# Kernel optimization log

Hardware: AMD Instinct MI355X
Metric: run time of the kernel (lower is better)

## Reference

```python
import jax, jax.numpy as jnp
import numpy as np

N, D, H, C = 100000, 128, 8, 16  # nodes, units=H*C, heads, per-head channels
E = 400000                        # edges per edge set (2 edge sets)
LN_EPS = 1e-3                     # keras LayerNormalization default epsilon


def setup_inputs() -> dict:
    key = jax.random.key(0)
    ks = jax.random.split(key, 16)
    def dense(k, i, o):
        return jax.random.normal(k, (i, o), jnp.float32) / np.float32(np.sqrt(i))
    return dict(
        x=jax.random.normal(ks[0], (N, D), jnp.float32),
        src0=jax.random.randint(ks[1], (E,), 0, N),
        dst0=jax.random.randint(ks[2], (E,), 0, N),
        src1=jax.random.randint(ks[3], (E,), 0, N),
        dst1=jax.random.randint(ks[4], (E,), 0, N),
        Wk=dense(ks[5], D, D), bk=jnp.zeros((D,), jnp.float32),
        Wm=dense(ks[6], D, D), bm=jnp.zeros((D,), jnp.float32),
        Wq=dense(ks[7], D, D), bq=jnp.zeros((D,), jnp.float32),
        Wa=dense(ks[8], D, D), ba=jnp.zeros((D,), jnp.float32),
        Watt0=jax.random.normal(ks[9], (H, C, C), jnp.float32) / np.float32(np.sqrt(C)),
        Wmsg0=jax.random.normal(ks[10], (H, C, C), jnp.float32) / np.float32(np.sqrt(C)),
        Watt1=jax.random.normal(ks[11], (H, C, C), jnp.float32) / np.float32(np.sqrt(C)),
        Wmsg1=jax.random.normal(ks[12], (H, C, C), jnp.float32) / np.float32(np.sqrt(C)),
        prior0=jnp.ones((H,), jnp.float32),
        prior1=jnp.ones((H,), jnp.float32),
        skip=jnp.ones((), jnp.float32),
        gamma=jnp.ones((D,), jnp.float32),
        beta=jnp.zeros((D,), jnp.float32),
    )


def reference(x, src0, dst0, src1, dst1, Wk, bk, Wm, bm, Wq, bq, Wa, ba,
              Watt0, Wmsg0, Watt1, Wmsg1, prior0, prior1, skip, gamma, beta):
    # Node-level projections, split per head: [N, H, C]
    k = (x @ Wk + bk).reshape(N, H, C)
    m = (x @ Wm + bm).reshape(N, H, C)
    q = (x @ Wq + bq).reshape(N, H, C)
    scale = 1.0 / jnp.sqrt(jnp.float32(C))

    def edge_terms(src, dst, Watt, Wmsg, prior):
        # per-edge-type relation projections of gathered sender keys/messages
        ke = jnp.einsum('ehk,hkl->ehl', k[src], Watt)          # [E, H, C]
        score = jnp.einsum('ehl,ehl->eh', ke, q[dst]) * prior * scale  # [E, H]
        msg = jnp.einsum('ehk,hkl->ehl', m[src], Wmsg)          # [E, H, C]
        return score, msg

    s0, m0 = edge_terms(src0, dst0, Watt0, Wmsg0, prior0)
    s1, m1 = edge_terms(src1, dst1, Watt1, Wmsg1, prior1)

    # Joint segment softmax over all incoming edges (both edge sets) per receiver
    scores = jnp.concatenate([s0, s1], axis=0)   # [2E, H]
    msgs = jnp.concatenate([m0, m1], axis=0)     # [2E, H, C]
    recv = jnp.concatenate([dst0, dst1], axis=0)

    smax = jax.ops.segment_max(scores, recv, num_segments=N)   # [N, H]
    ex = jnp.exp(scores - smax[recv])
    denom = jax.ops.segment_sum(ex, recv, num_segments=N)      # [N, H]
    d_e = denom[recv]
    attn = ex / jnp.where(d_e > 0, d_e, 1.0)                   # [2E, H]

    pooled = jax.ops.segment_sum(attn[:, :, None] * msgs, recv,
                                 num_segments=N).reshape(N, D)  # [N, D]

    # aggr(gelu(pooled)); weighted skip; layer norm
    h = jax.nn.gelu(pooled, approximate=False) @ Wa + ba
    alpha = jax.nn.sigmoid(skip)
    out = alpha * h + (1.0 - alpha) * x
    mu = jnp.mean(out, axis=-1, keepdims=True)
    var = jnp.var(out, axis=-1, keepdims=True)
    out = (out - mu) * jax.lax.rsqrt(var + LN_EPS) * gamma + beta
    return out
```

## Files before the change

kernel.cpp:

```cpp
#include <hip/hip_runtime.h>
#include <hip/hip_bf16.h>
#include <math.h>

#define N_NODES 100000
#define DIM 128
#define NH 8
#define NC 16
#define E_EDGES 400000
#define LN_EPS 1e-3f
#define SCAN_B 1024
#define PROJ_GRID 512

typedef __attribute__((ext_vector_type(8))) short short8v;
typedef __attribute__((ext_vector_type(4))) short short4v;
typedef __attribute__((ext_vector_type(4))) float float4v;

__device__ __forceinline__ short bf16bits(float v) {
    __hip_bfloat16 b = __float2bfloat16(v);
    return *(short*)&b;
}

__device__ __forceinline__ void bf2x2(unsigned v, float& a, float& b) {
    a = __uint_as_float(v << 16);
    b = __uint_as_float(v & 0xffff0000u);
}

__global__ __launch_bounds__(128) void fuse_weights(
    const float* __restrict__ Wk, const float* __restrict__ bk,
    const float* __restrict__ Wm, const float* __restrict__ bm,
    const float* __restrict__ Wq, const float* __restrict__ bq,
    const float* __restrict__ Wa, const float* __restrict__ ba,
    const float* __restrict__ Watt0, const float* __restrict__ Wmsg0,
    const float* __restrict__ Watt1, const float* __restrict__ Wmsg1,
    const float* __restrict__ prior0, const float* __restrict__ prior1,
    __hip_bfloat16* __restrict__ Wt, float* __restrict__ bias)
{
    const int c = blockIdx.x;
    const int d = threadIdx.x;
    const int sec = c >> 7, j = c & 127, h = j >> 4, l = j & 15;
    float v = 0.f, b = 0.f;
    if (sec == 0)      { v = Wk[d * DIM + j]; b = bk[j]; }
    else if (sec == 1) { v = Wm[d * DIM + j]; b = bm[j]; }
    else if (sec == 4) { v = Wa[d * DIM + j]; b = ba[j]; }
    else if (sec == 2 || sec == 3) {
        const float* W2 = (sec == 2) ? Watt0 : Watt1;
        float scale = ((sec == 2) ? prior0[h] : prior1[h]) * 0.25f;
        float s = 0.f, sb = 0.f;
        #pragma unroll
        for (int ll = 0; ll < NC; ++ll) {
            float w2 = W2[h * 256 + l * 16 + ll];
            s  = fmaf(Wq[d * DIM + h * 16 + ll], w2, s);
            sb = fmaf(bq[h * 16 + ll], w2, sb);
        }
        v = s * scale; b = sb * scale;
    } else {
        const float* W2 = (sec == 5) ? Wmsg0 : Wmsg1;
        v = ((d >> 4) == h) ? W2[h * 256 + (d & 15) * 16 + l] : 0.f;
        b = 0.f;
    }
    Wt[(size_t)c * DIM + d] = __float2bfloat16(v);
    if (d == 0) bias[c] = b;
}

__global__ __launch_bounds__(512) void proj_mfma(
    const float* __restrict__ x,
    const __hip_bfloat16* __restrict__ Wt,
    const float* __restrict__ bias,
    __hip_bfloat16* __restrict__ kmr,
    __hip_bfloat16* __restrict__ qe)
{
    __shared__ __align__(16) short xs[2][32 * DIM];
    const int tid = threadIdx.x;
    const int wave = tid >> 6, lane = tid & 63;
    const int quad = lane >> 4, mcol = lane & 15;
    const int nt = N_NODES / 32;

    short8v wf[4][4];
    float4v bv[4];
    #pragma unroll
    for (int s = 0; s < 4; ++s) {
        const int c0 = s * 128 + wave * 16;
        const short* wp = (const short*)Wt + (size_t)(c0 + mcol) * DIM + quad * 8;
        #pragma unroll
        for (int kb = 0; kb < 4; ++kb)
            wf[s][kb] = *(const short8v*)(wp + kb * 32);
        bv[s] = *(const float4v*)(bias + c0 + quad * 4);
    }

    const int srow = tid >> 4, sc8 = tid & 15;
    const int swz = ((sc8 ^ (srow & 7)) * 8);

    int t = blockIdx.x;
    if (t >= nt) return;

    float4v f0 = *(const float4v*)(x + (size_t)(t * 32 + srow) * DIM + sc8 * 8);
    float4v f1 = *(const float4v*)(x + (size_t)(t * 32 + srow) * DIM + sc8 * 8 + 4);
    {
        short8v sv;
        #pragma unroll
        for (int j = 0; j < 4; ++j) { sv[j] = bf16bits(f0[j]); sv[j + 4] = bf16bits(f1[j]); }
        *(short8v*)(xs[0] + srow * DIM + swz) = sv;
    }
    {
        int nn = t + PROJ_GRID;
        if (nn < nt) {
            f0 = *(const float4v*)(x + (size_t)(nn * 32 + srow) * DIM + sc8 * 8);
            f1 = *(const float4v*)(x + (size_t)(nn * 32 + srow) * DIM + sc8 * 8 + 4);
        }
    }

    int cur = 0;
    for (; t < nt; t += PROJ_GRID) {
        asm volatile("s_waitcnt lgkmcnt(0)" ::: "memory");
        __builtin_amdgcn_s_barrier();

        short8v b0[4], b1[4];
        #pragma unroll
        for (int kb = 0; kb < 4; ++kb) {
            const int ch = ((quad + kb * 4) ^ (mcol & 7)) * 8;
            b0[kb] = *(const short8v*)(xs[cur] + mcol * DIM + ch);
            b1[kb] = *(const short8v*)(xs[cur] + (mcol + 16) * DIM + ch);
        }

        const int r0 = t * 32;

        {
            float4v aK0 = {0.f,0.f,0.f,0.f}, aK1 = {0.f,0.f,0.f,0.f};
            float4v aM0 = {0.f,0.f,0.f,0.f}, aM1 = {0.f,0.f,0.f,0.f};
            #pragma unroll
            for (int kb = 0; kb < 4; ++kb) {
                aK0 = __builtin_amdgcn_mfma_f32_16x16x32_bf16(wf[0][kb], b0[kb], aK0, 0, 0, 0);
                aK1 = __builtin_amdgcn_mfma_f32_16x16x32_bf16(wf[0][kb], b1[kb], aK1, 0, 0, 0);
                aM0 = __builtin_amdgcn_mfma_f32_16x16x32_bf16(wf[1][kb], b0[kb], aM0, 0, 0, 0);
                aM1 = __builtin_amdgcn_mfma_f32_16x16x32_bf16(wf[1][kb], b1[kb], aM1, 0, 0, 0);
            }
            short8v o0, o1;
            #pragma unroll
            for (int g = 0; g < 4; ++g) {
                o0[g]     = bf16bits(aK0[g] + bv[0][g]);
                o0[g + 4] = bf16bits(aM0[g] + bv[1][g]);
                o1[g]     = bf16bits(aK1[g] + bv[0][g]);
                o1[g + 4] = bf16bits(aM1[g] + bv[1][g]);
            }
            short* dp = (short*)kmr + (size_t)(r0 + mcol) * 256
                      + (wave * 4 + quad) * 8;
            *(short8v*)dp              = o0;
            *(short8v*)(dp + 16 * 256) = o1;
        }

        #pragma unroll
        for (int e = 0; e < 2; ++e) {
            float4v a0v = {0.f,0.f,0.f,0.f}, a1v = {0.f,0.f,0.f,0.f};
            #pragma unroll
            for (int kb = 0; kb < 4; ++kb) {
                a0v = __builtin_amdgcn_mfma_f32_16x16x32_bf16(wf[2 + e][kb], b0[kb], a0v, 0, 0, 0);
                a1v = __builtin_amdgcn_mfma_f32_16x16x32_bf16(wf[2 + e][kb], b1[kb], a1v, 0, 0, 0);
            }
            short4v o0, o1;
            #pragma unroll
            for (int g = 0; g < 4; ++g) {
                o0[g] = bf16bits(a0v[g] + bv[2 + e][g]);
                o1[g] = bf16bits(a1v[g] + bv[2 + e][g]);
            }
            short* dp = (short*)qe + ((size_t)e * N_NODES + r0 + mcol) * DIM
                      + wave * 16 + quad * 4;
            *(short4v*)dp              = o0;
            *(short4v*)(dp + 16 * DIM) = o1;
        }

        int nn = t + PROJ_GRID;
        if (nn < nt) {
            short8v sv;
            #pragma unroll
            for (int j = 0; j < 4; ++j) { sv[j] = bf16bits(f0[j]); sv[j + 4] = bf16bits(f1[j]); }
            *(short8v*)(xs[cur ^ 1] + srow * DIM + swz) = sv;
            int n2 = nn + PROJ_GRID;
            if (n2 < nt) {
                f0 = *(const float4v*)(x + (size_t)(n2 * 32 + srow) * DIM + sc8 * 8);
                f1 = *(const float4v*)(x + (size_t)(n2 * 32 + srow) * DIM + sc8 * 8 + 4);
            }
        }
        cur ^= 1;
    }
}

__global__ __launch_bounds__(256) void hist_kernel(
    const int* __restrict__ dst0, const int* __restrict__ dst1,
    int* __restrict__ counts)
{
    int e = blockIdx.x * 256 + threadIdx.x;
    if (e < E_EDGES) atomicAdd(&counts[dst0[e]], 1);
    int e1 = e - E_EDGES;
    if (e1 >= 0 && e1 < E_EDGES) atomicAdd(&counts[dst1[e1]], 1);
}

__global__ __launch_bounds__(SCAN_B) void scanA_kernel(
    const int* __restrict__ counts, int* __restrict__ row_ptr,
    int* __restrict__ bsum)
{
    __shared__ int buf[2][SCAN_B];
    int i = blockIdx.x * SCAN_B + threadIdx.x;
    int v = (i < N_NODES) ? counts[i] : 0;
    int cur = 0;
    buf[0][threadIdx.x] = v;
    __syncthreads();
    #pragma unroll
    for (int off = 1; off < SCAN_B; off <<= 1) {
        int t = buf[cur][threadIdx.x];
        int add = (threadIdx.x >= off) ? buf[cur][threadIdx.x - off] : 0;
        buf[cur ^ 1][threadIdx.x] = t + add;
        cur ^= 1;
        __syncthreads();
    }
    int inc = buf[cur][threadIdx.x];
    if (i < N_NODES) row_ptr[i] = inc - v;
    if (threadIdx.x == SCAN_B - 1) bsum[blockIdx.x] = inc;
}

__global__ __launch_bounds__(128) void scanB_kernel(int* __restrict__ bsum, int nblocks)
{
    __shared__ int buf[2][128];
    int t = threadIdx.x;
    int v = (t < nblocks) ? bsum[t] : 0;
    buf[0][t] = v;
    __syncthreads();
    int cur = 0;
    #pragma unroll
    for (int off = 1; off < 128; off <<= 1) {
        int a = buf[cur][t];
        if (t >= off) a += buf[cur][t - off];
        buf[cur ^ 1][t] = a;
        cur ^= 1;
        __syncthreads();
    }
    if (t < nblocks) bsum[t] = buf[cur][t] - v;
}

__global__ __launch_bounds__(SCAN_B) void scanC_kernel(
    int* __restrict__ row_ptr, int* __restrict__ cursor,
    const int* __restrict__ bsum)
{
    int i = blockIdx.x * SCAN_B + threadIdx.x;
    if (i < N_NODES) {
        int r = row_ptr[i] + bsum[blockIdx.x];
        row_ptr[i] = r;
        cursor[i] = r;
    }
}

__global__ __launch_bounds__(256) void scatter_kernel(
    const int* __restrict__ src0, const int* __restrict__ dst0,
    const int* __restrict__ src1, const int* __restrict__ dst1,
    int* __restrict__ cursor, unsigned int* __restrict__ eidx)
{
    int e = blockIdx.x * 256 + threadIdx.x;
    if (e < E_EDGES) {
        int d = dst0[e];
        int pos = atomicAdd(&cursor[d], 1);
        eidx[pos] = (unsigned int)src0[e];
    }
    int e1 = e - E_EDGES;
    if (e1 >= 0 && e1 < E_EDGES) {
        int d = dst1[e1];
        int pos = atomicAdd(&cursor[d], 1);
        eidx[pos] = (unsigned int)src1[e1] | 0x80000000u;
    }
}

__global__ __launch_bounds__(256) void agg_kernel(
    const char* __restrict__ kmr,
    const uint2* __restrict__ qe,
    const int* __restrict__ row_ptr, const int* __restrict__ counts,
    const unsigned int* __restrict__ eidx,
    __hip_bfloat16* __restrict__ acc)
{
    const int wave = threadIdx.x >> 6, lane = threadIdx.x & 63;
    const int n = blockIdx.x * 4 + wave;
    if (n >= N_NODES) return;
    const int start = row_ptr[n], cnt = counts[n];
    const int hi = lane >> 5;
    const int glane = lane & 31;
    const unsigned g16 = (unsigned)glane << 4;

    uint2 qu0 = qe[(size_t)n * 32 + glane];
    uint2 qu1 = qe[((size_t)N_NODES + n) * 32 + glane];
    float q00, q01, q02, q03, q10, q11, q12, q13;
    bf2x2(qu0.x, q00, q01); bf2x2(qu0.y, q02, q03);
    bf2x2(qu1.x, q10, q11); bf2x2(qu1.y, q12, q13);

    float b0 = 0.f, b1 = 0.f, b2 = 0.f, b3 = 0.f;
    float c0 = 0.f, c1 = 0.f, c2 = 0.f, c3 = 0.f;
    float den = 0.f;

#define PAIR_ACC(u, s1)                                                      \
    {                                                                        \
        float k0, k1, k2, k3, m0, m1, m2, m3;                                \
        bf2x2((u).x, k0, k1); bf2x2((u).y, k2, k3);                          \
        bf2x2((u).z, m0, m1); bf2x2((u).w, m2, m3);                          \
        float qa = (s1) ? q10 : q00, qb = (s1) ? q11 : q01;                  \
        float qc = (s1) ? q12 : q02, qd = (s1) ? q13 : q03;                  \
        float p = fmaf(k3, qd, fmaf(k2, qc, fmaf(k1, qb, k0 * qa)));         \
        p += __shfl_xor(p, 1, 64);                                           \
        p += __shfl_xor(p, 2, 64);                                           \
        float e = __expf(p);                                                 \
        den += e;                                                            \
        float e0 = (s1) ? 0.f : e, e1s = (s1) ? e : 0.f;                     \
        b0 = fmaf(e0, m0, b0); b1 = fmaf(e0, m1, b1);                        \
        b2 = fmaf(e0, m2, b2); b3 = fmaf(e0, m3, b3);                        \
        c0 = fmaf(e1s, m0, c0); c1 = fmaf(e1s, m1, c1);                      \
        c2 = fmaf(e1s, m2, c2); c3 = fmaf(e1s, m3, c3);                      \
    }

    int i = 0;
    for (; i + 8 <= cnt; i += 8) {
        unsigned ra = eidx[start + i + hi];
        unsigned rb = eidx[start + i + 2 + hi];
        unsigned rc = eidx[start + i + 4 + hi];
        unsigned rd = eidx[start + i + 6 + hi];
        uint4 ua = *(const uint4*)(kmr + ((size_t)(ra & 0x7fffffffu) << 9 | g16));
        uint4 ub = *(const uint4*)(kmr + ((size_t)(rb & 0x7fffffffu) << 9 | g16));
        uint4 uc = *(const uint4*)(kmr + ((size_t)(rc & 0x7fffffffu) << 9 | g16));
        uint4 ud = *(const uint4*)(kmr + ((size_t)(rd & 0x7fffffffu) << 9 | g16));
        PAIR_ACC(ua, (ra >> 31));
        PAIR_ACC(ub, (rb >> 31));
        PAIR_ACC(uc, (rc >> 31));
        PAIR_ACC(ud, (rd >> 31));
    }
    for (; i + 2 <= cnt; i += 2) {
        unsigned ra = eidx[start + i + hi];
        uint4 ua = *(const uint4*)(kmr + ((size_t)(ra & 0x7fffffffu) << 9 | g16));
        PAIR_ACC(ua, (ra >> 31));
    }
    if (i < cnt) {
        unsigned ra = eidx[start + i];
        uint4 ua = *(const uint4*)(kmr + ((size_t)(ra & 0x7fffffffu) << 9 | g16));
        unsigned s1 = ra >> 31;
        float k0, k1, k2, k3, m0, m1, m2, m3;
        bf2x2(ua.x, k0, k1); bf2x2(ua.y, k2, k3);
        bf2x2(ua.z, m0, m1); bf2x2(ua.w, m2, m3);
        float qa = s1 ? q10 : q00, qb = s1 ? q11 : q01;
        float qc = s1 ? q12 : q02, qd = s1 ? q13 : q03;
        float p = fmaf(k3, qd, fmaf(k2, qc, fmaf(k1, qb, k0 * qa)));
        p += __shfl_xor(p, 1, 64);
        p += __shfl_xor(p, 2, 64);
        float e = hi ? 0.f : __expf(p);
        den += e;
        float e0 = s1 ? 0.f : e, e1s = s1 ? e : 0.f;
        b0 = fmaf(e0, m0, b0); b1 = fmaf(e0, m1, b1);
        b2 = fmaf(e0, m2, b2); b3 = fmaf(e0, m3, b3);
        c0 = fmaf(e1s, m0, c0); c1 = fmaf(e1s, m1, c1);
        c2 = fmaf(e1s, m2, c2); c3 = fmaf(e1s, m3, c3);
    }
#undef PAIR_ACC

    den += __shfl_xor(den, 32, 64);
    b0 += __shfl_xor(b0, 32, 64); b1 += __shfl_xor(b1, 32, 64);
    b2 += __shfl_xor(b2, 32, 64); b3 += __shfl_xor(b3, 32, 64);
    c0 += __shfl_xor(c0, 32, 64); c1 += __shfl_xor(c1, 32, 64);
    c2 += __shfl_xor(c2, 32, 64); c3 += __shfl_xor(c3, 32, 64);

    float inv = (den > 0.f) ? (1.f / den) : 0.f;
    short4v o;
    if (!hi) {
        o[0] = bf16bits(b0 * inv); o[1] = bf16bits(b1 * inv);
        o[2] = bf16bits(b2 * inv); o[3] = bf16bits(b3 * inv);
        *(short4v*)((short*)acc + (size_t)n * 256 + glane * 4) = o;
    } else {
        o[0] = bf16bits(c0 * inv); o[1] = bf16bits(c1 * inv);
        o[2] = bf16bits(c2 * inv); o[3] = bf16bits(c3 * inv);
        *(short4v*)((short*)acc + (size_t)n * 256 + 128 + glane * 4) = o;
    }
}

__global__ __launch_bounds__(256) void final_mfma(
    const __hip_bfloat16* __restrict__ acc,
    const __hip_bfloat16* __restrict__ Wt,
    const float* __restrict__ bias,
    const float* __restrict__ x,
    const float* __restrict__ skip, const float* __restrict__ gamma,
    const float* __restrict__ beta, float* __restrict__ out)
{
    __shared__ __align__(16) short Pl[32 * DIM];
    __shared__ float hs[32][DIM];
    const int wave = threadIdx.x >> 6, lane = threadIdx.x & 63;
    const int quad = lane >> 4, mcol = lane & 15;
    const int r0 = blockIdx.x * 32;

    short8v a0[8], a1[8];
    const short* pp0 = (const short*)acc + (size_t)(r0 + mcol) * 256 + quad * 8;
    const short* pp1 = pp0 + 16 * 256;
    #pragma unroll
    for (int kb = 0; kb < 8; ++kb) {
        a0[kb] = *(const short8v*)(pp0 + kb * 32);
        a1[kb] = *(const short8v*)(pp1 + kb * 32);
    }
    const float alpha = 1.f / (1.f + expf(-skip[0]));

    #pragma unroll
    for (int t = 0; t < 2; ++t) {
        const int c0 = wave * 32 + t * 16;
        const short* wp5 = (const short*)Wt + (size_t)(5 * 128 + c0 + mcol) * DIM + quad * 8;
        const short* wp6 = (const short*)Wt + (size_t)(6 * 128 + c0 + mcol) * DIM + quad * 8;
        float4v p0 = {0.f, 0.f, 0.f, 0.f};
        float4v p1 = {0.f, 0.f, 0.f, 0.f};
        #pragma unroll
        for (int kb = 0; kb < 4; ++kb) {
            short8v bfr = *(const short8v*)(wp5 + kb * 32);
            p0 = __builtin_amdgcn_mfma_f32_16x16x32_bf16(a0[kb], bfr, p0, 0, 0, 0);
            p1 = __builtin_amdgcn_mfma_f32_16x16x32_bf16(a1[kb], bfr, p1, 0, 0, 0);
        }
        #pragma unroll
        for (int kb = 0; kb < 4; ++kb) {
            short8v bfr = *(const short8v*)(wp6 + kb * 32);
            p0 = __builtin_amdgcn_mfma_f32_16x16x32_bf16(a0[kb + 4], bfr, p0, 0, 0, 0);
            p1 = __builtin_amdgcn_mfma_f32_16x16x32_bf16(a1[kb + 4], bfr, p1, 0, 0, 0);
        }
        const int cc = c0 + mcol;
        #pragma unroll
        for (int g = 0; g < 4; ++g) {
            int rA = quad * 4 + g, rB = rA + 16;
            float vA = p0[g], vB = p1[g];
            vA = 0.5f * vA * (1.f + erff(vA * 0.70710678118654752f));
            vB = 0.5f * vB * (1.f + erff(vB * 0.70710678118654752f));
            Pl[rA * DIM + (((cc >> 3) ^ (rA & 7)) << 3) + (cc & 7)] = bf16bits(vA);
            Pl[rB * DIM + (((cc >> 3) ^ (rB & 7)) << 3) + (cc & 7)] = bf16bits(vB);
        }
    }
    __syncthreads();

    short8v g0[4], g1[4];
    #pragma unroll
    for (int kb = 0; kb < 4; ++kb) {
        const int ch = quad + kb * 4;
        g0[kb] = *(const short8v*)(Pl + mcol * DIM + ((ch ^ (mcol & 7)) << 3));
        g1[kb] = *(const short8v*)(Pl + (mcol + 16) * DIM + ((ch ^ (mcol & 7)) << 3));
    }

    #pragma unroll
    for (int t = 0; t < 2; ++t) {
        const int c0 = wave * 32 + t * 16;
        const short* wp = (const short*)Wt + (size_t)(4 * 128 + c0 + mcol) * DIM + quad * 8;
        float4v acc0 = {0.f, 0.f, 0.f, 0.f};
        float4v acc1 = {0.f, 0.f, 0.f, 0.f};
        #pragma unroll
        for (int kb = 0; kb < 4; ++kb) {
            short8v bfr = *(const short8v*)(wp + kb * 32);
            acc0 = __builtin_amdgcn_mfma_f32_16x16x32_bf16(g0[kb], bfr, acc0, 0, 0, 0);
            acc1 = __builtin_amdgcn_mfma_f32_16x16x32_bf16(g1[kb], bfr, acc1, 0, 0, 0);
        }
        const float bcol = bias[512 + c0 + mcol];
        const int cc = c0 + mcol;
        const int rq = quad * 4;
        #pragma unroll
        for (int g = 0; g < 4; ++g) {
            int rA = rq + g, rB = rq + 16 + g;
            hs[rA][cc] = alpha * (acc0[g] + bcol)
                       + (1.f - alpha) * x[(size_t)(r0 + rA) * DIM + cc];
            hs[rB][cc] = alpha * (acc1[g] + bcol)
                       + (1.f - alpha) * x[(size_t)(r0 + rB) * DIM + cc];
        }
    }
    __syncthreads();

    float gam0 = gamma[lane], gam1 = gamma[lane + 64];
    float bet0 = beta[lane],  bet1 = beta[lane + 64];
    for (int r = wave; r < 32; r += 4) {
        int row = r0 + r;
        float v0 = hs[r][lane], v1 = hs[r][lane + 64];
        float s = v0 + v1, s2 = v0 * v0 + v1 * v1;
        #pragma unroll
        for (int off = 1; off < 64; off <<= 1) {
            s  += __shfl_xor(s,  off, 64);
            s2 += __shfl_xor(s2, off, 64);
        }
        float mu = s * (1.f / 128.f);
        float var = s2 * (1.f / 128.f) - mu * mu;
        float rstd = rsqrtf(var + LN_EPS);
        out[(size_t)row * DIM + lane]      = (v0 - mu) * rstd * gam0 + bet0;
        out[(size_t)row * DIM + lane + 64] = (v1 - mu) * rstd * gam1 + bet1;
    }
}

extern "C" void kernel_launch(void* const* d_in, const int* in_sizes, int n_in,
                              void* d_out, int out_size, void* d_ws, size_t ws_size,
                              hipStream_t stream) {
    const float* x     = (const float*)d_in[0];
    const int*   src0  = (const int*)d_in[1];
    const int*   dst0  = (const int*)d_in[2];
    const int*   src1  = (const int*)d_in[3];
    const int*   dst1  = (const int*)d_in[4];
    const float* Wk    = (const float*)d_in[5];
    const float* bk    = (const float*)d_in[6];
    const float* Wm    = (const float*)d_in[7];
    const float* bm    = (const float*)d_in[8];
    const float* Wq    = (const float*)d_in[9];
    const float* bq    = (const float*)d_in[10];
    const float* Wa    = (const float*)d_in[11];
    const float* ba    = (const float*)d_in[12];
    const float* Watt0 = (const float*)d_in[13];
    const float* Wmsg0 = (const float*)d_in[14];
    const float* Watt1 = (const float*)d_in[15];
    const float* Wmsg1 = (const float*)d_in[16];
    const float* prior0= (const float*)d_in[17];
    const float* prior1= (const float*)d_in[18];
    const float* skip  = (const float*)d_in[19];
    const float* gamma = (const float*)d_in[20];
    const float* beta  = (const float*)d_in[21];
    float* out = (float*)d_out;

    char* wsb = (char*)d_ws;
    __hip_bfloat16* Wt    = (__hip_bfloat16*)wsb;  wsb += (size_t)896 * DIM * 2;
    float* bias           = (float*)wsb;           wsb += 896 * 4;
    __hip_bfloat16* kmr   = (__hip_bfloat16*)wsb;  wsb += (size_t)N_NODES * 256 * 2;
    __hip_bfloat16* qe    = (__hip_bfloat16*)wsb;  wsb += (size_t)2 * N_NODES * DIM * 2;
    __hip_bfloat16* acc   = (__hip_bfloat16*)wsb;  wsb += (size_t)N_NODES * 256 * 2;
    int* counts  = (int*)wsb;                      wsb += (size_t)N_NODES * 4;
    int* row_ptr = (int*)wsb;                      wsb += (size_t)N_NODES * 4;
    int* cursor  = (int*)wsb;                      wsb += (size_t)N_NODES * 4;
    int* bsum    = (int*)wsb;                      wsb += 128 * 4;
    unsigned int* eidx = (unsigned int*)wsb;

    hipMemsetAsync(counts, 0, (size_t)N_NODES * 4, stream);

    const int scan_blocks = (N_NODES + SCAN_B - 1) / SCAN_B;
    const int edge_blocks = (2 * E_EDGES + 255) / 256;

    hist_kernel<<<dim3(edge_blocks), dim3(256), 0, stream>>>(dst0, dst1, counts);
    scanA_kernel<<<dim3(scan_blocks), dim3(SCAN_B), 0, stream>>>(counts, row_ptr, bsum);
    scanB_kernel<<<dim3(1), dim3(128), 0, stream>>>(bsum, scan_blocks);
    scanC_kernel<<<dim3(scan_blocks), dim3(SCAN_B), 0, stream>>>(row_ptr, cursor, bsum);
    scatter_kernel<<<dim3(edge_blocks), dim3(256), 0, stream>>>(
        src0, dst0, src1, dst1, cursor, eidx);

    fuse_weights<<<dim3(896), dim3(128), 0, stream>>>(
        Wk, bk, Wm, bm, Wq, bq, Wa, ba,
        Watt0, Wmsg0, Watt1, Wmsg1, prior0, prior1, Wt, bias);
    proj_mfma<<<dim3(PROJ_GRID), dim3(512), 0, stream>>>(
        x, Wt, bias, kmr, qe);

    agg_kernel<<<dim3((N_NODES + 3) / 4), dim3(256), 0, stream>>>(
        (const char*)kmr, (const uint2*)qe, row_ptr, counts, eidx, acc);

    final_mfma<<<dim3(N_NODES / 32), dim3(256), 0, stream>>>(
        acc, Wt, bias, x, skip, gamma, beta, out);
}
```

Measured before the change: 393.6 us.

## Apply per-head message weights and GELU inside aggregation kernel

The per-edge-set message projection (Wmsg0/Wmsg1) moves out of the final MFMA kernel and into the end of the aggregation kernel, where each wave computes a small per-head matvec on its pooled accumulators using packed bf16 weights loaded from a new tiny prep kernel. GELU is applied there too, so the aggregation output shrinks from 256 to 128 bf16 values per node. This halves the intermediate write and read traffic and removes one MFMA stage plus the LDS round trip in the final kernel. In exchange it adds shuffles, register pressure and scalar FMA work to the aggregation kernel.

```diff
diff --git a/kernel.cpp b/kernel.cpp
--- a/kernel.cpp
+++ b/kernel.cpp
@@ -30,8 +30,7 @@
     const float* __restrict__ Wm, const float* __restrict__ bm,
     const float* __restrict__ Wq, const float* __restrict__ bq,
     const float* __restrict__ Wa, const float* __restrict__ ba,
-    const float* __restrict__ Watt0, const float* __restrict__ Wmsg0,
-    const float* __restrict__ Watt1, const float* __restrict__ Wmsg1,
+    const float* __restrict__ Watt0, const float* __restrict__ Watt1,
     const float* __restrict__ prior0, const float* __restrict__ prior1,
     __hip_bfloat16* __restrict__ Wt, float* __restrict__ bias)
 {
@@ -42,7 +41,7 @@
     if (sec == 0)      { v = Wk[d * DIM + j]; b = bk[j]; }
     else if (sec == 1) { v = Wm[d * DIM + j]; b = bm[j]; }
     else if (sec == 4) { v = Wa[d * DIM + j]; b = ba[j]; }
-    else if (sec == 2 || sec == 3) {
+    else {
         const float* W2 = (sec == 2) ? Watt0 : Watt1;
         float scale = ((sec == 2) ? prior0[h] : prior1[h]) * 0.25f;
         float s = 0.f, sb = 0.f;
@@ -53,13 +52,30 @@
             sb = fmaf(bq[h * 16 + ll], w2, sb);
         }
         v = s * scale; b = sb * scale;
-    } else {
-        const float* W2 = (sec == 5) ? Wmsg0 : Wmsg1;
-        v = ((d >> 4) == h) ? W2[h * 256 + (d & 15) * 16 + l] : 0.f;
-        b = 0.f;
     }
     Wt[(size_t)c * DIM + d] = __float2bfloat16(v);
     if (d == 0) bias[c] = b;
+}
+
+__global__ __launch_bounds__(256) void fuse_wmt(
+    const float* __restrict__ Wmsg0, const float* __restrict__ Wmsg1,
+    unsigned* __restrict__ wmt)
+{
+    const int tid = threadIdx.x;
+    const int row = tid >> 2;
+    const int s = row >> 5, g = row & 31;
+    const int h = g >> 2, lb = (g & 3) * 4;
+    const float* W = s ? Wmsg1 : Wmsg0;
+    #pragma unroll
+    for (int jj = 0; jj < 8; ++jj) {
+        int j = (tid & 3) * 8 + jj;
+        int k2 = j >> 2, li = j & 3, l = lb + li;
+        float wlo = W[h * 256 + (2 * k2) * 16 + l];
+        float whi = W[h * 256 + (2 * k2 + 1) * 16 + l];
+        unsigned pk = ((unsigned)(unsigned short)bf16bits(wlo))
+                    | ((unsigned)(unsigned short)bf16bits(whi) << 16);
+        wmt[row * 32 + j] = pk;
+    }
 }
 
 __global__ __launch_bounds__(512) void proj_mfma(
@@ -270,9 +286,10 @@
 __global__ __launch_bounds__(256) void agg_kernel(
     const char* __restrict__ kmr,
     const uint2* __restrict__ qe,
+    const unsigned* __restrict__ wmt,
     const int* __restrict__ row_ptr, const int* __restrict__ counts,
     const unsigned int* __restrict__ eidx,
-    __hip_bfloat16* __restrict__ acc)
+    uint2* __restrict__ pooled)
 {
     const int wave = threadIdx.x >> 6, lane = threadIdx.x & 63;
     const int n = blockIdx.x * 4 + wave;
@@ -358,39 +375,88 @@
     b2 += __shfl_xor(b2, 32, 64); b3 += __shfl_xor(b3, 32, 64);
     c0 += __shfl_xor(c0, 32, 64); c1 += __shfl_xor(c1, 32, 64);
     c2 += __shfl_xor(c2, 32, 64); c3 += __shfl_xor(c3, 32, 64);
-
     float inv = (den > 0.f) ? (1.f / den) : 0.f;
-    short4v o;
+
+    uint4 wv[8];
+    {
+        const uint4* wrow = (const uint4*)(wmt + (size_t)(hi * 32 + glane) * 32);
+        #pragma unroll
+        for (int j = 0; j < 8; ++j) wv[j] = wrow[j];
+    }
+#define WMR(idx) ( ((idx) & 3) == 0 ? wv[(idx) >> 2].x :                     \
+                   ((idx) & 3) == 1 ? wv[(idx) >> 2].y :                     \
+                   ((idx) & 3) == 2 ? wv[(idx) >> 2].z : wv[(idx) >> 2].w )
+
+    float t0 = hi ? c0 : b0, t1 = hi ? c1 : b1;
+    float t2 = hi ? c2 : b2, t3 = hi ? c3 : b3;
+    float u0 = __shfl_xor(t0, 1, 64), u1 = __shfl_xor(t1, 1, 64);
+    float u2 = __shfl_xor(t2, 1, 64), u3 = __shfl_xor(t3, 1, 64);
+    const bool pb0 = (glane & 1);
+    float A0 = pb0 ? u0 : t0, A1 = pb0 ? u1 : t1, A2 = pb0 ? u2 : t2, A3 = pb0 ? u3 : t3;
+    float A4 = pb0 ? t0 : u0, A5 = pb0 ? t1 : u1, A6 = pb0 ? t2 : u2, A7 = pb0 ? t3 : u3;
+    float B0 = __shfl_xor(A0, 2, 64), B1 = __shfl_xor(A1, 2, 64);
+    float B2 = __shfl_xor(A2, 2, 64), B3 = __shfl_xor(A3, 2, 64);
+    float B4 = __shfl_xor(A4, 2, 64), B5 = __shfl_xor(A5, 2, 64);
+    float B6 = __shfl_xor(A6, 2, 64), B7 = __shfl_xor(A7, 2, 64);
+    const bool pb1 = (glane & 2);
+    float h0 = pb1 ? B0 : A0, h1 = pb1 ? B1 : A1, h2 = pb1 ? B2 : A2, h3 = pb1 ? B3 : A3;
+    float h4 = pb1 ? B4 : A4, h5 = pb1 ? B5 : A5, h6 = pb1 ? B6 : A6, h7 = pb1 ? B7 : A7;
+    float h8 = pb1 ? A0 : B0, h9 = pb1 ? A1 : B1, h10 = pb1 ? A2 : B2, h11 = pb1 ? A3 : B3;
+    float h12 = pb1 ? A4 : B4, h13 = pb1 ? A5 : B5, h14 = pb1 ? A6 : B6, h15 = pb1 ? A7 : B7;
+
+    float o0 = 0.f, o1 = 0.f, o2 = 0.f, o3 = 0.f;
+#define MV(k2, clo, chi_)                                                    \
+    { float wl, wh;                                                          \
+      bf2x2(WMR((k2) * 4 + 0), wl, wh);                                      \
+      o0 = fmaf(chi_, wh, fmaf(clo, wl, o0));                                \
+      bf2x2(WMR((k2) * 4 + 1), wl, wh);                                      \
+      o1 = fmaf(chi_, wh, fmaf(clo, wl, o1));                                \
+      bf2x2(WMR((k2) * 4 + 2), wl, wh);                                      \
+      o2 = fmaf(chi_, wh, fmaf(clo, wl, o2));                                \
+      bf2x2(WMR((k2) * 4 + 3), wl, wh);                                      \
+      o3 = fmaf(chi_, wh, fmaf(clo, wl, o3)); }
+    MV(0, h0, h1)   MV(1, h2, h3)   MV(2, h4, h5)   MV(3, h6, h7)
+    MV(4, h8, h9)   MV(5, h10, h11) MV(6, h12, h13) MV(7, h14, h15)
+#undef MV
+#undef WMR
+
+    o0 += __shfl_xor(o0, 32, 64);
+    o1 += __shfl_xor(o1, 32, 64);
+    o2 += __shfl_xor(o2, 32, 64);
+    o3 += __shfl_xor(o3, 32, 64);
+    o0 *= inv; o1 *= inv; o2 *= inv; o3 *= inv;
+    o0 = 0.5f * o0 * (1.f + erff(o0 * 0.70710678118654752f));
+    o1 = 0.5f * o1 * (1.f + erff(o1 * 0.70710678118654752f));
+    o2 = 0.5f * o2 * (1.f + erff(o2 * 0.70710678118654752f));
+    o3 = 0.5f * o3 * (1.f + erff(o3 * 0.70710678118654752f));
     if (!hi) {
-        o[0] = bf16bits(b0 * inv); o[1] = bf16bits(b1 * inv);
-        o[2] = bf16bits(b2 * inv); o[3] = bf16bits(b3 * inv);
-        *(short4v*)((short*)acc + (size_t)n * 256 + glane * 4) = o;
-    } else {
-        o[0] = bf16bits(c0 * inv); o[1] = bf16bits(c1 * inv);
-        o[2] = bf16bits(c2 * inv); o[3] = bf16bits(c3 * inv);
-        *(short4v*)((short*)acc + (size_t)n * 256 + 128 + glane * 4) = o;
+        uint2 o;
+        o.x = ((unsigned)(unsigned short)bf16bits(o0))
+            | ((unsigned)(unsigned short)bf16bits(o1) << 16);
+        o.y = ((unsigned)(unsigned short)bf16bits(o2))
+            | ((unsigned)(unsigned short)bf16bits(o3) << 16);
+        pooled[(size_t)n * 32 + glane] = o;
     }
 }
 
 __global__ __launch_bounds__(256) void final_mfma(
-    const __hip_bfloat16* __restrict__ acc,
+    const __hip_bfloat16* __restrict__ pooled,
     const __hip_bfloat16* __restrict__ Wt,
     const float* __restrict__ bias,
     const float* __restrict__ x,
     const float* __restrict__ skip, const float* __restrict__ gamma,
     const float* __restrict__ beta, float* __restrict__ out)
 {
-    __shared__ __align__(16) short Pl[32 * DIM];
     __shared__ float hs[32][DIM];
     const int wave = threadIdx.x >> 6, lane = threadIdx.x & 63;
     const int quad = lane >> 4, mcol = lane & 15;
     const int r0 = blockIdx.x * 32;
 
-    short8v a0[8], a1[8];
-    const short* pp0 = (const short*)acc + (size_t)(r0 + mcol) * 256 + quad * 8;
-    const short* pp1 = pp0 + 16 * 256;
+    short8v a0[4], a1[4];
+    const short* pp0 = (const short*)pooled + (size_t)(r0 + mcol) * DIM + quad * 8;
+    const short* pp1 = pp0 + 16 * DIM;
     #pragma unroll
-    for (int kb = 0; kb < 8; ++kb) {
+    for (int kb = 0; kb < 4; ++kb) {
         a0[kb] = *(const short8v*)(pp0 + kb * 32);
         a1[kb] = *(const short8v*)(pp1 + kb * 32);
     }
@@ -399,54 +465,14 @@
     #pragma unroll
     for (int t = 0; t < 2; ++t) {
         const int c0 = wave * 32 + t * 16;
-        const short* wp5 = (const short*)Wt + (size_t)(5 * 128 + c0 + mcol) * DIM + quad * 8;
-        const short* wp6 = (const short*)Wt + (size_t)(6 * 128 + c0 + mcol) * DIM + quad * 8;
-        float4v p0 = {0.f, 0.f, 0.f, 0.f};
-        float4v p1 = {0.f, 0.f, 0.f, 0.f};
-        #pragma unroll
-        for (int kb = 0; kb < 4; ++kb) {
-            short8v bfr = *(const short8v*)(wp5 + kb * 32);
-            p0 = __builtin_amdgcn_mfma_f32_16x16x32_bf16(a0[kb], bfr, p0, 0, 0, 0);
-            p1 = __builtin_amdgcn_mfma_f32_16x16x32_bf16(a1[kb], bfr, p1, 0, 0, 0);
-        }
-        #pragma unroll
-        for (int kb = 0; kb < 4; ++kb) {
-            short8v bfr = *(const short8v*)(wp6 + kb * 32);
-            p0 = __builtin_amdgcn_mfma_f32_16x16x32_bf16(a0[kb + 4], bfr, p0, 0, 0, 0);
-            p1 = __builtin_amdgcn_mfma_f32_16x16x32_bf16(a1[kb + 4], bfr, p1, 0, 0, 0);
-        }
-        const int cc = c0 + mcol;
-        #pragma unroll
-        for (int g = 0; g < 4; ++g) {
-            int rA = quad * 4 + g, rB = rA + 16;
-            float vA = p0[g], vB = p1[g];
-            vA = 0.5f * vA * (1.f + erff(vA * 0.70710678118654752f));
-            vB = 0.5f * vB * (1.f + erff(vB * 0.70710678118654752f));
-            Pl[rA * DIM + (((cc >> 3) ^ (rA & 7)) << 3) + (cc & 7)] = bf16bits(vA);
-            Pl[rB * DIM + (((cc >> 3) ^ (rB & 7)) << 3) + (cc & 7)] = bf16bits(vB);
-        }
-    }
-    __syncthreads();
-
-    short8v g0[4], g1[4];
-    #pragma unroll
-    for (int kb = 0; kb < 4; ++kb) {
-        const int ch = quad + kb * 4;
-        g0[kb] = *(const short8v*)(Pl + mcol * DIM + ((ch ^ (mcol & 7)) << 3));
-        g1[kb] = *(const short8v*)(Pl + (mcol + 16) * DIM + ((ch ^ (mcol & 7)) << 3));
-    }
-
-    #pragma unroll
-    for (int t = 0; t < 2; ++t) {
-        const int c0 = wave * 32 + t * 16;
-        const short* wp = (const short*)Wt + (size_t)(4 * 128 + c0 + mcol) * DIM + quad * 8;
+        const short* wp = (const short*)Wt + (size_t)(512 + c0 + mcol) * DIM + quad * 8;
         float4v acc0 = {0.f, 0.f, 0.f, 0.f};
         float4v acc1 = {0.f, 0.f, 0.f, 0.f};
         #pragma unroll
         for (int kb = 0; kb < 4; ++kb) {
             short8v bfr = *(const short8v*)(wp + kb * 32);
-            acc0 = __builtin_amdgcn_mfma_f32_16x16x32_bf16(g0[kb], bfr, acc0, 0, 0, 0);
-            acc1 = __builtin_amdgcn_mfma_f32_16x16x32_bf16(g1[kb], bfr, acc1, 0, 0, 0);
+            acc0 = __builtin_amdgcn_mfma_f32_16x16x32_bf16(a0[kb], bfr, acc0, 0, 0, 0);
+            acc1 = __builtin_amdgcn_mfma_f32_16x16x32_bf16(a1[kb], bfr, acc1, 0, 0, 0);
         }
         const float bcol = bias[512 + c0 + mcol];
         const int cc = c0 + mcol;
@@ -509,11 +535,12 @@
     float* out = (float*)d_out;
 
     char* wsb = (char*)d_ws;
-    __hip_bfloat16* Wt    = (__hip_bfloat16*)wsb;  wsb += (size_t)896 * DIM * 2;
-    float* bias           = (float*)wsb;           wsb += 896 * 4;
+    __hip_bfloat16* Wt    = (__hip_bfloat16*)wsb;  wsb += (size_t)640 * DIM * 2;
+    float* bias           = (float*)wsb;           wsb += 640 * 4;
+    unsigned* wmt         = (unsigned*)wsb;        wsb += 2048 * 4;
     __hip_bfloat16* kmr   = (__hip_bfloat16*)wsb;  wsb += (size_t)N_NODES * 256 * 2;
     __hip_bfloat16* qe    = (__hip_bfloat16*)wsb;  wsb += (size_t)2 * N_NODES * DIM * 2;
-    __hip_bfloat16* acc   = (__hip_bfloat16*)wsb;  wsb += (size_t)N_NODES * 256 * 2;
+    __hip_bfloat16* pooled= (__hip_bfloat16*)wsb;  wsb += (size_t)N_NODES * DIM * 2;
     int* counts  = (int*)wsb;                      wsb += (size_t)N_NODES * 4;
     int* row_ptr = (int*)wsb;                      wsb += (size_t)N_NODES * 4;
     int* cursor  = (int*)wsb;                      wsb += (size_t)N_NODES * 4;
@@ -532,15 +559,17 @@
     scatter_kernel<<<dim3(edge_blocks), dim3(256), 0, stream>>>(
         src0, dst0, src1, dst1, cursor, eidx);
 
-    fuse_weights<<<dim3(896), dim3(128), 0, stream>>>(
+    fuse_weights<<<dim3(640), dim3(128), 0, stream>>>(
         Wk, bk, Wm, bm, Wq, bq, Wa, ba,
-        Watt0, Wmsg0, Watt1, Wmsg1, prior0, prior1, Wt, bias);
+        Watt0, Watt1, prior0, prior1, Wt, bias);
+    fuse_wmt<<<dim3(1), dim3(256), 0, stream>>>(Wmsg0, Wmsg1, wmt);
     proj_mfma<<<dim3(PROJ_GRID), dim3(512), 0, stream>>>(
         x, Wt, bias, kmr, qe);
 
     agg_kernel<<<dim3((N_NODES + 3) / 4), dim3(256), 0, stream>>>(
-        (const char*)kmr, (const uint2*)qe, row_ptr, counts, eidx, acc);
+        (const char*)kmr, (const uint2*)qe, wmt, row_ptr, counts, eidx,
+        (uint2*)pooled);
 
     final_mfma<<<dim3(N_NODES / 32), dim3(256), 0, stream>>>(
-        acc, Wt, bias, x, skip, gamma, beta, out);
-}
+        pooled, Wt, bias, x, skip, gamma, beta, out);
+}
```

New measurement: 415.8 us. 1.06x slower.
